# Kernel optimization log

Measured on AMD Instinct MI355X. Metric: run time of the kernel, lower is better.

## Reference

```python
import jax, jax.numpy as jnp
import numpy as np

B, S, HID = 2, 2048, 1024
H, HKV, D = 8, 2, 256
G = H // HKV            # GQA group size = 4
RD = D // 4             # partial rotary dim = 64
BASE = 10000000.0
EPS = 1e-6


def _rmsnorm(x, w):
    # x: [..., D]; matches QwenRMSNorm (fp32 math)
    xf = x.astype(jnp.float32)
    var = jnp.mean(xf * xf, axis=-1, keepdims=True)
    return w * (xf * jax.lax.rsqrt(var + EPS)).astype(x.dtype)


def _rotate_half(x):
    h = x.shape[-1] // 2
    return jnp.concatenate([-x[..., h:], x[..., :h]], axis=-1)


def _rope_cos_sin(position_ids, dtype):
    inv_freq = 1.0 / (BASE ** (jnp.arange(0, RD, 2, dtype=jnp.float32) / RD))
    freqs = position_ids.astype(jnp.float32)[:, None] * inv_freq[None, :]  # [S, RD/2]
    emb = jnp.concatenate([freqs, freqs], axis=-1)                          # [S, RD]
    return jnp.cos(emb).astype(dtype)[None, None], jnp.sin(emb).astype(dtype)[None, None]


def setup_inputs() -> dict:
    key = jax.random.key(0)
    ks = jax.random.split(key, 8)
    sc = lambda fan_in: 1.0 / np.sqrt(fan_in)
    return {
        "hidden_states": jax.random.normal(ks[0], (B, S, HID), jnp.float32),
        "position_ids": jnp.arange(S, dtype=jnp.int32),
        "Wq": jax.random.normal(ks[1], (H * D * 2, HID), jnp.float32) * sc(HID),
        "Wk": jax.random.normal(ks[2], (HKV * D, HID), jnp.float32) * sc(HID),
        "Wv": jax.random.normal(ks[3], (HKV * D, HID), jnp.float32) * sc(HID),
        "Wo": jax.random.normal(ks[4], (HID, H * D), jnp.float32) * sc(H * D),
        "q_norm_w": jnp.ones((D,), jnp.float32),
        "k_norm_w": jnp.ones((D,), jnp.float32),
    }


def reference(hidden_states, position_ids, Wq, Wk, Wv, Wo, q_norm_w, k_norm_w):
    b, s, _ = hidden_states.shape
    q_and_gate = hidden_states @ Wq.T                      # [B,S,2*H*D]
    q = q_and_gate[..., : H * D]
    gate = q_and_gate[..., H * D :]
    k = hidden_states @ Wk.T                               # [B,S,HKV*D]
    v = hidden_states @ Wv.T

    q = _rmsnorm(q.reshape(b, s, H, D), q_norm_w).transpose(0, 2, 1, 3)    # [B,H,S,D]
    k = _rmsnorm(k.reshape(b, s, HKV, D), k_norm_w).transpose(0, 2, 1, 3)  # [B,HKV,S,D]
    v = v.reshape(b, s, HKV, D).transpose(0, 2, 1, 3)                       # [B,HKV,S,D]

    cos, sin = _rope_cos_sin(position_ids, q.dtype)        # [1,1,S,RD]
    q_rot, q_pass = q[..., :RD], q[..., RD:]
    k_rot, k_pass = k[..., :RD], k[..., RD:]
    q = jnp.concatenate([q_rot * cos + _rotate_half(q_rot) * sin, q_pass], axis=-1)
    k = jnp.concatenate([k_rot * cos + _rotate_half(k_rot) * sin, k_pass], axis=-1)

    # GQA: group q heads by kv head instead of repeat_interleave (same math)
    qg = q.reshape(b, HKV, G, s, D)
    scale = 1.0 / np.sqrt(D).astype(np.float32)
    scores = jnp.einsum('bhgqd,bhkd->bhgqk', qg, k) * scale  # [B,HKV,G,S,S]
    attn = jax.nn.softmax(scores, axis=-1)                   # NOTE: no causal mask (as in source)
    out = jnp.einsum('bhgqk,bhkd->bhgqd', attn, v)           # [B,HKV,G,S,D]
    out = out.reshape(b, H, s, D).transpose(0, 2, 1, 3).reshape(b, s, H * D)

    out = out * jax.nn.silu(gate)
    return out @ Wo.T
```

## Files before the change

kernel.cpp:

```cpp
#include <hip/hip_runtime.h>
#include <math.h>

typedef unsigned short u16;
typedef unsigned int   u32;
typedef __attribute__((ext_vector_type(4))) float f32x4;
typedef __attribute__((ext_vector_type(8))) short s16x8;
typedef __attribute__((ext_vector_type(4))) unsigned short u16x4;

#define B_N   2
#define S_N   2048
#define HID_N 1024
#define H_N   8
#define HKV_N 2
#define D_N   256
#define QKVW  5120

__device__ __forceinline__ u16 f2bf(float f) {
  union { float f; u32 u; } x; x.f = f;
  u32 r = x.u + 0x7FFFu + ((x.u >> 16) & 1u);
  return (u16)(r >> 16);
}
__device__ __forceinline__ float bf2f(u16 u) {
  union { u32 u; float f; } x; x.u = ((u32)u) << 16; return x.f;
}
__device__ __forceinline__ void gload_lds16(const u16* g, u16* l) {
  __builtin_amdgcn_global_load_lds((const __attribute__((address_space(1))) u32*)g,
                                   (__attribute__((address_space(3))) u32*)l, 16, 0, 0);
}

__global__ __launch_bounds__(256)
void cast_bf16_kernel(const float* __restrict__ src, u16* __restrict__ dst, int n4) {
  int i = blockIdx.x * blockDim.x + threadIdx.x;
  int stride = gridDim.x * blockDim.x;
  for (; i < n4; i += stride) {
    float4 v = reinterpret_cast<const float4*>(src)[i];
    u16x4 o;
    o.x = f2bf(v.x); o.y = f2bf(v.y); o.z = f2bf(v.z); o.w = f2bf(v.w);
    reinterpret_cast<u16x4*>(dst)[i] = o;
  }
}

__global__ __launch_bounds__(256)
void trig_kernel(const int* __restrict__ pos, float* __restrict__ ct, float* __restrict__ st) {
  int i = blockIdx.x * blockDim.x + threadIdx.x;
  if (i >= S_N * 32) return;
  int s = i >> 5, j = i & 31;
  double inv = exp(-(double)j * (log(1.0e7) / 32.0));
  double ang = (double)pos[s] * inv;
  ct[i] = (float)cos(ang);
  st[i] = (float)sin(ang);
}

template <int OUT_BF16>
__global__ __launch_bounds__(256, 2)
void gemm_bt_kernel(const u16* __restrict__ A, const u16* __restrict__ Bw,
                    void* __restrict__ Cout, int M, int N, int K) {
  const int nbn = N >> 7;
  const int bm = blockIdx.x / nbn;
  const int bn = blockIdx.x % nbn;
  const int tid = threadIdx.x;
  const int lane = tid & 63;
  const int wr = tid >> 7;
  const int wc = (tid >> 6) & 1;
  __shared__ u16 sA[2][128 * 32];
  __shared__ u16 sB[2][128 * 32];
  f32x4 acc[4][4] = {};
  const u16* Ab = A + (size_t)(bm << 7) * K;
  const u16* Bb = Bw + (size_t)(bn << 7) * K;
  const int r_st = tid >> 2;
  const int c_st = (tid & 3) * 8;
  const int nkt = K >> 5;

  auto stage = [&](int buf, int kt) {
    const int k0 = kt << 5;
    gload_lds16(Ab + (size_t)r_st * K + k0 + c_st,        &sA[buf][tid * 8]);
    gload_lds16(Ab + (size_t)(r_st + 64) * K + k0 + c_st, &sA[buf][2048 + tid * 8]);
    gload_lds16(Bb + (size_t)r_st * K + k0 + c_st,        &sB[buf][tid * 8]);
    gload_lds16(Bb + (size_t)(r_st + 64) * K + k0 + c_st, &sB[buf][2048 + tid * 8]);
  };

  stage(0, 0);
  int cur = 0;
  const int ra = (wr << 6) + (lane & 15);
  const int rb = (wc << 6) + (lane & 15);
  const int ks = (lane >> 4) << 3;
  for (int kt = 0; kt < nkt; ++kt) {
    asm volatile("s_waitcnt vmcnt(0)" ::: "memory");
    __syncthreads();
    if (kt + 1 < nkt) stage(cur ^ 1, kt + 1);
    const u16* sa = sA[cur];
    const u16* sb = sB[cur];
    s16x8 af[4], bfr[4];
#pragma unroll
    for (int m = 0; m < 4; ++m) af[m] = *reinterpret_cast<const s16x8*>(sa + (ra + m * 16) * 32 + ks);
#pragma unroll
    for (int n = 0; n < 4; ++n) bfr[n] = *reinterpret_cast<const s16x8*>(sb + (rb + n * 16) * 32 + ks);
#pragma unroll
    for (int m = 0; m < 4; ++m)
#pragma unroll
      for (int n = 0; n < 4; ++n)
        acc[m][n] = __builtin_amdgcn_mfma_f32_16x16x32_bf16(af[m], bfr[n], acc[m][n], 0, 0, 0);
    cur ^= 1;
  }
  const int row0 = (bm << 7) + (wr << 6) + ((lane >> 4) << 2);
  const int col0 = (bn << 7) + (wc << 6) + (lane & 15);
#pragma unroll
  for (int m = 0; m < 4; ++m)
#pragma unroll
    for (int n = 0; n < 4; ++n)
#pragma unroll
      for (int j = 0; j < 4; ++j) {
        size_t idx = (size_t)(row0 + m * 16 + j) * N + col0 + n * 16;
        if (OUT_BF16) ((u16*)Cout)[idx] = f2bf(acc[m][n][j]);
        else          ((float*)Cout)[idx] = acc[m][n][j];
      }
}

__global__ __launch_bounds__(256)
void normrope_kernel(const u16* __restrict__ qkv, const float* __restrict__ qw,
                     const float* __restrict__ kw, const float* __restrict__ ct,
                     const float* __restrict__ st, u16* __restrict__ q_r,
                     u16* __restrict__ k_r) {
  const int lane = threadIdx.x & 63;
  const int row = blockIdx.x * 4 + (threadIdx.x >> 6);
  const int nq = B_N * S_N * H_N;
  const u16* src; u16* dst; const float* w;
  int s;
  if (row < nq) {
    int h = row & 7; int bs = row >> 3; s = bs & (S_N - 1); int b = bs >> 11;
    src = qkv + (size_t)(b * S_N + s) * QKVW + h * 256;
    dst = q_r + ((size_t)(b * H_N + h) * S_N + s) * 256;
    w = qw;
  } else {
    int r2 = row - nq;
    int h = r2 & 1; int bs = r2 >> 1; s = bs & (S_N - 1); int b = bs >> 11;
    src = qkv + (size_t)(b * S_N + s) * QKVW + 4096 + h * 256;
    dst = k_r + ((size_t)(b * HKV_N + h) * S_N + s) * 256;
    w = kw;
  }
  u16x4 xv = *reinterpret_cast<const u16x4*>(src + lane * 4);
  float x0 = bf2f(xv.x), x1 = bf2f(xv.y), x2 = bf2f(xv.z), x3 = bf2f(xv.w);
  float ss = x0 * x0 + x1 * x1 + x2 * x2 + x3 * x3;
#pragma unroll
  for (int off = 1; off < 64; off <<= 1) ss += __shfl_xor(ss, off);
  float rinv = rsqrtf(ss * (1.0f / 256.0f) + 1e-6f);
  float4 wv = *reinterpret_cast<const float4*>(w + lane * 4);
  float y[4] = { x0 * rinv * wv.x, x1 * rinv * wv.y, x2 * rinv * wv.z, x3 * rinv * wv.w };
  float p[4];
  p[0] = __shfl_xor(y[0], 8);
  p[1] = __shfl_xor(y[1], 8);
  p[2] = __shfl_xor(y[2], 8);
  p[3] = __shfl_xor(y[3], 8);
  if (lane < 16) {
    const float sgn = (lane < 8) ? -1.0f : 1.0f;
    const int jb = (lane * 4) & 31;
#pragma unroll
    for (int e = 0; e < 4; ++e) {
      float c = ct[(size_t)s * 32 + jb + e];
      float sn = st[(size_t)s * 32 + jb + e];
      y[e] = y[e] * c + sgn * p[e] * sn;
    }
  }
  u16x4 ov;
  ov.x = f2bf(y[0]); ov.y = f2bf(y[1]); ov.z = f2bf(y[2]); ov.w = f2bf(y[3]);
  *reinterpret_cast<u16x4*>(dst + lane * 4) = ov;
}

__global__ __launch_bounds__(256)
void vtrans_kernel(const u16* __restrict__ qkv, u16* __restrict__ vt) {
  const int bid = blockIdx.x;
  const int dt = bid & 3;
  const int stile = (bid >> 2) & 31;
  const int bh = bid >> 7;
  const int b = bh >> 1, kvh = bh & 1;
  __shared__ u16 tile[64][68];
  const int t = threadIdx.x;
  const u16* src = qkv + (size_t)(b * S_N + stile * 64) * QKVW + 4608 + kvh * 256 + dt * 64;
#pragma unroll
  for (int i = 0; i < 2; ++i) {
    int sl = i * 32 + (t >> 3);
    int d8 = (t & 7) * 8;
    s16x8 v = *reinterpret_cast<const s16x8*>(src + (size_t)sl * QKVW + d8);
    u16x4 lo = { (u16)v[0], (u16)v[1], (u16)v[2], (u16)v[3] };
    u16x4 hi = { (u16)v[4], (u16)v[5], (u16)v[6], (u16)v[7] };
    *reinterpret_cast<u16x4*>(&tile[sl][d8]) = lo;
    *reinterpret_cast<u16x4*>(&tile[sl][d8 + 4]) = hi;
  }
  __syncthreads();
#pragma unroll
  for (int i = 0; i < 2; ++i) {
    int dl = i * 32 + (t >> 3);
    int s8 = (t & 7) * 8;
    u16 tmp[8];
#pragma unroll
    for (int e = 0; e < 8; ++e) tmp[e] = tile[s8 + e][dl];
    u16x4 lo = { tmp[0], tmp[1], tmp[2], tmp[3] };
    u16x4 hi = { tmp[4], tmp[5], tmp[6], tmp[7] };
    u16* dstp = vt + ((size_t)(bh * 256 + dt * 64 + dl)) * S_N + stile * 64 + s8;
    *reinterpret_cast<u16x4*>(dstp) = lo;
    *reinterpret_cast<u16x4*>(dstp + 4) = hi;
  }
}

__global__ __launch_bounds__(512, 2)
void attn_kernel(const u16* __restrict__ q_r, const u16* __restrict__ k_r,
                 const u16* __restrict__ vt, const u16* __restrict__ qkv,
                 u16* __restrict__ act) {
  const int dd = blockIdx.x;
  const int xcd = dd & 7;
  const int idx = dd >> 3;
  const int combo = xcd >> 1;
  const int within = (xcd & 1) * 32 + idx;
  const int b = combo >> 1;
  const int kvh = combo & 1;
  const int h = kvh * 4 + (within >> 4);
  const int qt = within & 15;

  const int tid = threadIdx.x;
  const int lane = tid & 63;
  const int wv = tid >> 6;
  const int l15 = lane & 15;
  const int l4 = lane >> 4;

  __shared__ u16 sK[2][64 * 256];
  __shared__ u16 sVt[2][256 * 64];
  __shared__ u16 sP[8][16 * 64];

  const int q0 = qt * 128 + wv * 16;
  const u16* qb = q_r + ((size_t)(b * H_N + h) * S_N + q0) * 256;
  s16x8 qf[8];
#pragma unroll
  for (int kk = 0; kk < 8; ++kk)
    qf[kk] = *reinterpret_cast<const s16x8*>(qb + (size_t)l15 * 256 + kk * 32 + l4 * 8);

  f32x4 oacc[16] = {};
  float mrow[4] = { -1e30f, -1e30f, -1e30f, -1e30f };
  float lrow[4] = { 0.f, 0.f, 0.f, 0.f };

  const u16* kbase = k_r + ((size_t)(b * HKV_N + kvh) * S_N) * 256;
  const u16* vbase = vt + ((size_t)(b * HKV_N + kvh) * 256) * S_N;

  const int krow_b = tid >> 5;
  const int kp = tid & 31;
  const int vrow_b = tid >> 3;
  const int vp = tid & 7;

  auto stageKV = [&](int buf, int step) {
    const int kv0 = step << 6;
#pragma unroll
    for (int i = 0; i < 4; ++i) {
      const int krow = i * 16 + krow_b;
      gload_lds16(kbase + (size_t)(kv0 + krow) * 256 + ((kp ^ (krow_b & 7)) << 3),
                  &sK[buf][i * 4096 + tid * 8]);
    }
#pragma unroll
    for (int i = 0; i < 4; ++i) {
      const int vrow = i * 64 + vrow_b;
      gload_lds16(vbase + (size_t)vrow * S_N + kv0 + ((vp ^ (vrow_b & 7)) << 3),
                  &sVt[buf][i * 4096 + tid * 8]);
    }
  };

  stageKV(0, 0);
  int cur = 0;
  const float scale = 0.0625f;
  const int sw = (l15 & 7);
  for (int step = 0; step < 32; ++step) {
    asm volatile("s_waitcnt vmcnt(0)" ::: "memory");
    __syncthreads();
    if (step + 1 < 32) stageKV(cur ^ 1, step + 1);
    const u16* ktile = sK[cur];
    const u16* vtile = sVt[cur];

    f32x4 sacc[4] = {};
#pragma unroll
    for (int kk = 0; kk < 8; ++kk) {
      const int slot = kk * 4 + l4;
#pragma unroll
      for (int g = 0; g < 4; ++g) {
        const int row = g * 16 + l15;
        s16x8 kf = *reinterpret_cast<const s16x8*>(ktile + row * 256 + ((slot ^ sw) << 3));
        sacc[g] = __builtin_amdgcn_mfma_f32_16x16x32_bf16(qf[kk], kf, sacc[g], 0, 0, 0);
      }
    }

    float sc[16];
#pragma unroll
    for (int g = 0; g < 4; ++g)
#pragma unroll
      for (int j = 0; j < 4; ++j) sc[g * 4 + j] = sacc[g][j] * scale;
    float vmax[4];
#pragma unroll
    for (int j = 0; j < 4; ++j) {
      float v = fmaxf(fmaxf(sc[j], sc[4 + j]), fmaxf(sc[8 + j], sc[12 + j]));
      v = fmaxf(v, __shfl_xor(v, 1));
      v = fmaxf(v, __shfl_xor(v, 2));
      v = fmaxf(v, __shfl_xor(v, 4));
      v = fmaxf(v, __shfl_xor(v, 8));
      vmax[j] = v;
    }
    float grow = fmaxf(fmaxf(vmax[0] - mrow[0], vmax[1] - mrow[1]),
                       fmaxf(vmax[2] - mrow[2], vmax[3] - mrow[3]));
    if (__any(grow > 0.0f)) {
      float alpha[4];
#pragma unroll
      for (int j = 0; j < 4; ++j) {
        float mnew = fmaxf(mrow[j], vmax[j]);
        alpha[j] = __expf(mrow[j] - mnew);
        mrow[j] = mnew;
        lrow[j] *= alpha[j];
      }
#pragma unroll
      for (int nf = 0; nf < 16; ++nf) {
        oacc[nf][0] *= alpha[0]; oacc[nf][1] *= alpha[1];
        oacc[nf][2] *= alpha[2]; oacc[nf][3] *= alpha[3];
      }
    }
    float p[16];
#pragma unroll
    for (int g = 0; g < 4; ++g)
#pragma unroll
      for (int j = 0; j < 4; ++j) p[g * 4 + j] = __expf(sc[g * 4 + j] - mrow[j]);
#pragma unroll
    for (int j = 0; j < 4; ++j) {
      float r = (p[j] + p[4 + j]) + (p[8 + j] + p[12 + j]);
      r += __shfl_xor(r, 1);
      r += __shfl_xor(r, 2);
      r += __shfl_xor(r, 4);
      r += __shfl_xor(r, 8);
      lrow[j] += r;
    }

    u16* pl = &sP[wv][0];
#pragma unroll
    for (int g = 0; g < 4; ++g)
#pragma unroll
      for (int j = 0; j < 4; ++j) {
        const int row = l4 * 4 + j;
        const int col = g * 16 + l15;
        pl[row * 64 + ((((col >> 3) ^ (row & 7)) << 3) | (col & 7))] = f2bf(p[g * 4 + j]);
      }
    asm volatile("s_waitcnt lgkmcnt(0)" ::: "memory");
    __builtin_amdgcn_sched_barrier(0);

#pragma unroll
    for (int chunk = 0; chunk < 2; ++chunk) {
      s16x8 paf = *reinterpret_cast<const s16x8*>(
          pl + l15 * 64 + (((chunk * 4 + l4) ^ sw) << 3));
#pragma unroll
      for (int nf = 0; nf < 16; ++nf) {
        const int d = nf * 16 + l15;
        s16x8 vf = *reinterpret_cast<const s16x8*>(
            vtile + d * 64 + (((chunk * 4 + l4) ^ sw) << 3));
        oacc[nf] = __builtin_amdgcn_mfma_f32_16x16x32_bf16(paf, vf, oacc[nf], 0, 0, 0);
      }
    }
    cur ^= 1;
  }

  float invl[4];
#pragma unroll
  for (int j = 0; j < 4; ++j) invl[j] = 1.0f / lrow[j];
#pragma unroll
  for (int nf = 0; nf < 16; ++nf) {
#pragma unroll
    for (int j = 0; j < 4; ++j) {
      const int srow = q0 + l4 * 4 + j;
      const int d = nf * 16 + l15;
      float o = oacc[nf][j] * invl[j];
      float g = bf2f(qkv[(size_t)(b * S_N + srow) * QKVW + 2048 + h * 256 + d]);
      float sg = g / (1.0f + __expf(-g));
      act[(size_t)(b * S_N + srow) * 2048 + h * 256 + d] = f2bf(o * sg);
    }
  }
}

extern "C" void kernel_launch(void* const* d_in, const int* in_sizes, int n_in,
                              void* d_out, int out_size, void* d_ws, size_t ws_size,
                              hipStream_t stream) {
  const float* hs  = (const float*)d_in[0];
  const int*   pos = (const int*)d_in[1];
  const float* Wq  = (const float*)d_in[2];
  const float* Wk  = (const float*)d_in[3];
  const float* Wv  = (const float*)d_in[4];
  const float* Wo  = (const float*)d_in[5];
  const float* qw  = (const float*)d_in[6];
  const float* kw  = (const float*)d_in[7];
  float* out = (float*)d_out;

  char* w8 = (char*)d_ws;
  u16* hs_bf   = (u16*)(w8);
  u16* wqkv_bf = (u16*)(w8 + 8388608);
  u16* wo_bf   = (u16*)(w8 + 18874368);
  u16* qkv_raw = (u16*)(w8 + 23068672);
  u16* q_r     = (u16*)(w8 + 65011712);
  u16* k_r     = (u16*)(w8 + 81788928);
  u16* vt      = (u16*)(w8 + 85983232);
  u16* act     = (u16*)(w8 + 90177536);
  float* cost  = (float*)(w8 + 106954752);
  float* sint  = (float*)(w8 + 107216896);

  auto cast_launch = [&](const float* src, u16* dst, int n) {
    int n4 = n >> 2;
    int blocks = (n4 + 255) / 256;
    if (blocks > 2048) blocks = 2048;
    cast_bf16_kernel<<<blocks, 256, 0, stream>>>(src, dst, n4);
  };
  cast_launch(hs, hs_bf, B_N * S_N * HID_N);
  cast_launch(Wq, wqkv_bf, 4096 * 1024);
  cast_launch(Wk, wqkv_bf + 4194304, 512 * 1024);
  cast_launch(Wv, wqkv_bf + 4718592, 512 * 1024);
  cast_launch(Wo, wo_bf, 1024 * 2048);

  trig_kernel<<<(S_N * 32) / 256, 256, 0, stream>>>(pos, cost, sint);

  gemm_bt_kernel<1><<<32 * 40, 256, 0, stream>>>(hs_bf, wqkv_bf, (void*)qkv_raw, 4096, 5120, 1024);

  normrope_kernel<<<(B_N * S_N * (H_N + HKV_N)) / 4, 256, 0, stream>>>(
      qkv_raw, qw, kw, cost, sint, q_r, k_r);
  vtrans_kernel<<<512, 256, 0, stream>>>(qkv_raw, vt);

  attn_kernel<<<256, 512, 0, stream>>>(q_r, k_r, vt, qkv_raw, act);

  gemm_bt_kernel<0><<<32 * 8, 256, 0, stream>>>(act, wo_bf, (void*)out, 4096, 1024, 2048);
}
```

Measured before the change: 256.4 us.

## Restructure attention blocks so each wave covers one GQA head with 32 query rows

Each attention block now holds 4 waves, one per query head of a KV group, and each wave processes 32 query rows (two 16-row groups) over a shared 32-row query tile. Each K/V fragment read from LDS now feeds two MFMAs, which halves LDS read traffic per MFMA. MFMA sections are also wrapped in s_setprio raises. In exchange, per-thread registers double (oacc 2x16 accumulators) and occupancy drops to a single 256-thread block per CU, which reduces latency hiding.

```diff
diff --git a/kernel.cpp b/kernel.cpp
--- a/kernel.cpp
+++ b/kernel.cpp
@@ -202,7 +202,7 @@
   }
 }
 
-__global__ __launch_bounds__(512, 2)
+__global__ __launch_bounds__(256, 1)
 void attn_kernel(const u16* __restrict__ q_r, const u16* __restrict__ k_r,
                  const u16* __restrict__ vt, const u16* __restrict__ qkv,
                  u16* __restrict__ act) {
@@ -210,61 +210,66 @@
   const int xcd = dd & 7;
   const int idx = dd >> 3;
   const int combo = xcd >> 1;
-  const int within = (xcd & 1) * 32 + idx;
+  const int qt = (xcd & 1) * 32 + idx;
   const int b = combo >> 1;
   const int kvh = combo & 1;
-  const int h = kvh * 4 + (within >> 4);
-  const int qt = within & 15;
 
   const int tid = threadIdx.x;
   const int lane = tid & 63;
   const int wv = tid >> 6;
+  const int h = kvh * 4 + wv;
   const int l15 = lane & 15;
   const int l4 = lane >> 4;
 
   __shared__ u16 sK[2][64 * 256];
   __shared__ u16 sVt[2][256 * 64];
-  __shared__ u16 sP[8][16 * 64];
-
-  const int q0 = qt * 128 + wv * 16;
+  __shared__ u16 sP[4][32 * 64];
+
+  const int q0 = qt * 32;
   const u16* qb = q_r + ((size_t)(b * H_N + h) * S_N + q0) * 256;
-  s16x8 qf[8];
-#pragma unroll
-  for (int kk = 0; kk < 8; ++kk)
-    qf[kk] = *reinterpret_cast<const s16x8*>(qb + (size_t)l15 * 256 + kk * 32 + l4 * 8);
-
-  f32x4 oacc[16] = {};
-  float mrow[4] = { -1e30f, -1e30f, -1e30f, -1e30f };
-  float lrow[4] = { 0.f, 0.f, 0.f, 0.f };
+  s16x8 qf[2][8];
+#pragma unroll
+  for (int rg = 0; rg < 2; ++rg)
+#pragma unroll
+    for (int kk = 0; kk < 8; ++kk)
+      qf[rg][kk] = *reinterpret_cast<const s16x8*>(
+          qb + (size_t)(rg * 16 + l15) * 256 + kk * 32 + l4 * 8);
+
+  f32x4 oacc[2][16] = {};
+  float mrow[2][4], lrow[2][4];
+#pragma unroll
+  for (int rg = 0; rg < 2; ++rg)
+#pragma unroll
+    for (int j = 0; j < 4; ++j) { mrow[rg][j] = -1e30f; lrow[rg][j] = 0.f; }
 
   const u16* kbase = k_r + ((size_t)(b * HKV_N + kvh) * S_N) * 256;
   const u16* vbase = vt + ((size_t)(b * HKV_N + kvh) * 256) * S_N;
 
-  const int krow_b = tid >> 5;
-  const int kp = tid & 31;
-  const int vrow_b = tid >> 3;
-  const int vp = tid & 7;
+  const int k_sc = tid & 31;
+  const int k_rb = tid >> 5;
+  const int v_sc = tid & 7;
+  const int v_rb = (tid >> 3) & 7;
 
   auto stageKV = [&](int buf, int step) {
     const int kv0 = step << 6;
 #pragma unroll
-    for (int i = 0; i < 4; ++i) {
-      const int krow = i * 16 + krow_b;
-      gload_lds16(kbase + (size_t)(kv0 + krow) * 256 + ((kp ^ (krow_b & 7)) << 3),
-                  &sK[buf][i * 4096 + tid * 8]);
-    }
-#pragma unroll
-    for (int i = 0; i < 4; ++i) {
-      const int vrow = i * 64 + vrow_b;
-      gload_lds16(vbase + (size_t)vrow * S_N + kv0 + ((vp ^ (vrow_b & 7)) << 3),
-                  &sVt[buf][i * 4096 + tid * 8]);
+    for (int i = 0; i < 8; ++i) {
+      const int row = i * 8 + k_rb;
+      gload_lds16(kbase + (size_t)(kv0 + row) * 256 + ((k_sc ^ k_rb) << 3),
+                  &sK[buf][i * 2048 + tid * 8]);
+    }
+#pragma unroll
+    for (int i = 0; i < 8; ++i) {
+      const int rowd = i * 32 + (tid >> 3);
+      gload_lds16(vbase + (size_t)rowd * S_N + kv0 + ((v_sc ^ v_rb) << 3),
+                  &sVt[buf][i * 2048 + tid * 8]);
     }
   };
 
   stageKV(0, 0);
   int cur = 0;
   const float scale = 0.0625f;
-  const int sw = (l15 & 7);
+  const int sw = l15 & 7;
   for (int step = 0; step < 32; ++step) {
     asm volatile("s_waitcnt vmcnt(0)" ::: "memory");
     __syncthreads();
@@ -272,107 +277,135 @@
     const u16* ktile = sK[cur];
     const u16* vtile = sVt[cur];
 
-    f32x4 sacc[4] = {};
+    f32x4 sacc[2][4] = {};
+    __builtin_amdgcn_s_setprio(1);
 #pragma unroll
     for (int kk = 0; kk < 8; ++kk) {
       const int slot = kk * 4 + l4;
 #pragma unroll
       for (int g = 0; g < 4; ++g) {
-        const int row = g * 16 + l15;
-        s16x8 kf = *reinterpret_cast<const s16x8*>(ktile + row * 256 + ((slot ^ sw) << 3));
-        sacc[g] = __builtin_amdgcn_mfma_f32_16x16x32_bf16(qf[kk], kf, sacc[g], 0, 0, 0);
-      }
-    }
-
-    float sc[16];
-#pragma unroll
-    for (int g = 0; g < 4; ++g)
-#pragma unroll
-      for (int j = 0; j < 4; ++j) sc[g * 4 + j] = sacc[g][j] * scale;
-    float vmax[4];
-#pragma unroll
-    for (int j = 0; j < 4; ++j) {
-      float v = fmaxf(fmaxf(sc[j], sc[4 + j]), fmaxf(sc[8 + j], sc[12 + j]));
-      v = fmaxf(v, __shfl_xor(v, 1));
-      v = fmaxf(v, __shfl_xor(v, 2));
-      v = fmaxf(v, __shfl_xor(v, 4));
-      v = fmaxf(v, __shfl_xor(v, 8));
-      vmax[j] = v;
-    }
-    float grow = fmaxf(fmaxf(vmax[0] - mrow[0], vmax[1] - mrow[1]),
-                       fmaxf(vmax[2] - mrow[2], vmax[3] - mrow[3]));
+        s16x8 kf = *reinterpret_cast<const s16x8*>(
+            ktile + (g * 16 + l15) * 256 + ((slot ^ sw) << 3));
+        sacc[0][g] = __builtin_amdgcn_mfma_f32_16x16x32_bf16(qf[0][kk], kf, sacc[0][g], 0, 0, 0);
+        sacc[1][g] = __builtin_amdgcn_mfma_f32_16x16x32_bf16(qf[1][kk], kf, sacc[1][g], 0, 0, 0);
+      }
+    }
+    __builtin_amdgcn_s_setprio(0);
+
+    float sc[2][16];
+#pragma unroll
+    for (int rg = 0; rg < 2; ++rg)
+#pragma unroll
+      for (int g = 0; g < 4; ++g)
+#pragma unroll
+        for (int j = 0; j < 4; ++j) sc[rg][g * 4 + j] = sacc[rg][g][j] * scale;
+    float vmax[2][4];
+#pragma unroll
+    for (int rg = 0; rg < 2; ++rg)
+#pragma unroll
+      for (int j = 0; j < 4; ++j) {
+        float v = fmaxf(fmaxf(sc[rg][j], sc[rg][4 + j]),
+                        fmaxf(sc[rg][8 + j], sc[rg][12 + j]));
+        v = fmaxf(v, __shfl_xor(v, 1));
+        v = fmaxf(v, __shfl_xor(v, 2));
+        v = fmaxf(v, __shfl_xor(v, 4));
+        v = fmaxf(v, __shfl_xor(v, 8));
+        vmax[rg][j] = v;
+      }
+    float grow = -1.f;
+#pragma unroll
+    for (int rg = 0; rg < 2; ++rg)
+#pragma unroll
+      for (int j = 0; j < 4; ++j) grow = fmaxf(grow, vmax[rg][j] - mrow[rg][j]);
     if (__any(grow > 0.0f)) {
-      float alpha[4];
+#pragma unroll
+      for (int rg = 0; rg < 2; ++rg) {
+        float alpha[4];
+#pragma unroll
+        for (int j = 0; j < 4; ++j) {
+          float mnew = fmaxf(mrow[rg][j], vmax[rg][j]);
+          alpha[j] = __expf(mrow[rg][j] - mnew);
+          mrow[rg][j] = mnew;
+          lrow[rg][j] *= alpha[j];
+        }
+#pragma unroll
+        for (int nf = 0; nf < 16; ++nf) {
+          oacc[rg][nf][0] *= alpha[0]; oacc[rg][nf][1] *= alpha[1];
+          oacc[rg][nf][2] *= alpha[2]; oacc[rg][nf][3] *= alpha[3];
+        }
+      }
+    }
+    float p[2][16];
+#pragma unroll
+    for (int rg = 0; rg < 2; ++rg) {
+#pragma unroll
+      for (int g = 0; g < 4; ++g)
+#pragma unroll
+        for (int j = 0; j < 4; ++j)
+          p[rg][g * 4 + j] = __expf(sc[rg][g * 4 + j] - mrow[rg][j]);
 #pragma unroll
       for (int j = 0; j < 4; ++j) {
-        float mnew = fmaxf(mrow[j], vmax[j]);
-        alpha[j] = __expf(mrow[j] - mnew);
-        mrow[j] = mnew;
-        lrow[j] *= alpha[j];
-      }
-#pragma unroll
-      for (int nf = 0; nf < 16; ++nf) {
-        oacc[nf][0] *= alpha[0]; oacc[nf][1] *= alpha[1];
-        oacc[nf][2] *= alpha[2]; oacc[nf][3] *= alpha[3];
-      }
-    }
-    float p[16];
-#pragma unroll
-    for (int g = 0; g < 4; ++g)
-#pragma unroll
-      for (int j = 0; j < 4; ++j) p[g * 4 + j] = __expf(sc[g * 4 + j] - mrow[j]);
-#pragma unroll
-    for (int j = 0; j < 4; ++j) {
-      float r = (p[j] + p[4 + j]) + (p[8 + j] + p[12 + j]);
-      r += __shfl_xor(r, 1);
-      r += __shfl_xor(r, 2);
-      r += __shfl_xor(r, 4);
-      r += __shfl_xor(r, 8);
-      lrow[j] += r;
+        float r = (p[rg][j] + p[rg][4 + j]) + (p[rg][8 + j] + p[rg][12 + j]);
+        r += __shfl_xor(r, 1);
+        r += __shfl_xor(r, 2);
+        r += __shfl_xor(r, 4);
+        r += __shfl_xor(r, 8);
+        lrow[rg][j] += r;
+      }
     }
 
     u16* pl = &sP[wv][0];
 #pragma unroll
-    for (int g = 0; g < 4; ++g)
-#pragma unroll
-      for (int j = 0; j < 4; ++j) {
-        const int row = l4 * 4 + j;
-        const int col = g * 16 + l15;
-        pl[row * 64 + ((((col >> 3) ^ (row & 7)) << 3) | (col & 7))] = f2bf(p[g * 4 + j]);
-      }
+    for (int rg = 0; rg < 2; ++rg)
+#pragma unroll
+      for (int g = 0; g < 4; ++g)
+#pragma unroll
+        for (int j = 0; j < 4; ++j) {
+          const int row = rg * 16 + l4 * 4 + j;
+          const int col = g * 16 + l15;
+          pl[row * 64 + ((((col >> 3) ^ (row & 7)) << 3) | (col & 7))] = f2bf(p[rg][g * 4 + j]);
+        }
     asm volatile("s_waitcnt lgkmcnt(0)" ::: "memory");
     __builtin_amdgcn_sched_barrier(0);
 
-#pragma unroll
-    for (int chunk = 0; chunk < 2; ++chunk) {
-      s16x8 paf = *reinterpret_cast<const s16x8*>(
-          pl + l15 * 64 + (((chunk * 4 + l4) ^ sw) << 3));
+    __builtin_amdgcn_s_setprio(1);
+#pragma unroll
+    for (int c = 0; c < 2; ++c) {
+      s16x8 paf[2];
+#pragma unroll
+      for (int rg = 0; rg < 2; ++rg)
+        paf[rg] = *reinterpret_cast<const s16x8*>(
+            pl + (rg * 16 + l15) * 64 + (((c * 4 + l4) ^ sw) << 3));
 #pragma unroll
       for (int nf = 0; nf < 16; ++nf) {
+        s16x8 vf = *reinterpret_cast<const s16x8*>(
+            vtile + (nf * 16 + l15) * 64 + (((c * 4 + l4) ^ sw) << 3));
+        oacc[0][nf] = __builtin_amdgcn_mfma_f32_16x16x32_bf16(paf[0], vf, oacc[0][nf], 0, 0, 0);
+        oacc[1][nf] = __builtin_amdgcn_mfma_f32_16x16x32_bf16(paf[1], vf, oacc[1][nf], 0, 0, 0);
+      }
+    }
+    __builtin_amdgcn_s_setprio(0);
+    cur ^= 1;
+  }
+
+  float invl[2][4];
+#pragma unroll
+  for (int rg = 0; rg < 2; ++rg)
+#pragma unroll
+    for (int j = 0; j < 4; ++j) invl[rg][j] = 1.0f / lrow[rg][j];
+#pragma unroll
+  for (int rg = 0; rg < 2; ++rg)
+#pragma unroll
+    for (int nf = 0; nf < 16; ++nf)
+#pragma unroll
+      for (int j = 0; j < 4; ++j) {
+        const int srow = q0 + rg * 16 + l4 * 4 + j;
         const int d = nf * 16 + l15;
-        s16x8 vf = *reinterpret_cast<const s16x8*>(
-            vtile + d * 64 + (((chunk * 4 + l4) ^ sw) << 3));
-        oacc[nf] = __builtin_amdgcn_mfma_f32_16x16x32_bf16(paf, vf, oacc[nf], 0, 0, 0);
-      }
-    }
-    cur ^= 1;
-  }
-
-  float invl[4];
-#pragma unroll
-  for (int j = 0; j < 4; ++j) invl[j] = 1.0f / lrow[j];
-#pragma unroll
-  for (int nf = 0; nf < 16; ++nf) {
-#pragma unroll
-    for (int j = 0; j < 4; ++j) {
-      const int srow = q0 + l4 * 4 + j;
-      const int d = nf * 16 + l15;
-      float o = oacc[nf][j] * invl[j];
-      float g = bf2f(qkv[(size_t)(b * S_N + srow) * QKVW + 2048 + h * 256 + d]);
-      float sg = g / (1.0f + __expf(-g));
-      act[(size_t)(b * S_N + srow) * 2048 + h * 256 + d] = f2bf(o * sg);
-    }
-  }
+        float o = oacc[rg][nf][j] * invl[rg][j];
+        float g = bf2f(qkv[(size_t)(b * S_N + srow) * QKVW + 2048 + h * 256 + d]);
+        float sg = g / (1.0f + __expf(-g));
+        act[(size_t)(b * S_N + srow) * 2048 + h * 256 + d] = f2bf(o * sg);
+      }
 }
 
 extern "C" void kernel_launch(void* const* d_in, const int* in_sizes, int n_in,
@@ -420,7 +453,7 @@
       qkv_raw, qw, kw, cost, sint, q_r, k_r);
   vtrans_kernel<<<512, 256, 0, stream>>>(qkv_raw, vt);
 
-  attn_kernel<<<256, 512, 0, stream>>>(q_r, k_r, vt, qkv_raw, act);
+  attn_kernel<<<256, 256, 0, stream>>>(q_r, k_r, vt, qkv_raw, act);
 
   gemm_bt_kernel<0><<<32 * 8, 256, 0, stream>>>(act, wo_bf, (void*)out, 4096, 1024, 2048);
 }
```

Result: slower. 314.0 us (+22.5%).

## Transpose QK^T MFMA operands so each lane owns one query row for softmax

Applied to the files above, without the earlier changes.

Swaps the MFMA operand order in the score computation so the score tile is transposed and each lane holds scores for a single query row across 16 key columns. Row max and row sum then need only two cross-lane shuffles instead of four shuffles per row for four rows, and the running max and sum collapse to scalars. P is packed with v_cvt_pk_bf16_f32 and written as 8-byte vector stores through a new swizzle, and the scale is folded into an fma inside the exp. Rescale factors and the final normalizer are broadcast back to the accumulator layout with __shfl, which adds some cross-lane traffic.

```diff
diff --git a/kernel.cpp b/kernel.cpp
--- a/kernel.cpp
+++ b/kernel.cpp
@@ -22,6 +22,11 @@
 }
 __device__ __forceinline__ float bf2f(u16 u) {
   union { u32 u; float f; } x; x.u = ((u32)u) << 16; return x.f;
+}
+__device__ __forceinline__ u32 pk_bf16(float lo, float hi) {
+  u32 r;
+  asm("v_cvt_pk_bf16_f32 %0, %1, %2" : "=v"(r) : "v"(lo), "v"(hi));
+  return r;
 }
 __device__ __forceinline__ void gload_lds16(const u16* g, u16* l) {
   __builtin_amdgcn_global_load_lds((const __attribute__((address_space(1))) u32*)g,
@@ -234,8 +239,8 @@
     qf[kk] = *reinterpret_cast<const s16x8*>(qb + (size_t)l15 * 256 + kk * 32 + l4 * 8);
 
   f32x4 oacc[16] = {};
-  float mrow[4] = { -1e30f, -1e30f, -1e30f, -1e30f };
-  float lrow[4] = { 0.f, 0.f, 0.f, 0.f };
+  float mrow = -1e30f;
+  float lrow = 0.f;
 
   const u16* kbase = k_r + ((size_t)(b * HKV_N + kvh) * S_N) * 256;
   const u16* vbase = vt + ((size_t)(b * HKV_N + kvh) * 256) * S_N;
@@ -264,7 +269,8 @@
   stageKV(0, 0);
   int cur = 0;
   const float scale = 0.0625f;
-  const int sw = (l15 & 7);
+  const int sw = l15 & 7;
+  const int swp = l15 & 14;
   for (int step = 0; step < 32; ++step) {
     asm volatile("s_waitcnt vmcnt(0)" ::: "memory");
     __syncthreads();
@@ -278,96 +284,83 @@
       const int slot = kk * 4 + l4;
 #pragma unroll
       for (int g = 0; g < 4; ++g) {
-        const int row = g * 16 + l15;
-        s16x8 kf = *reinterpret_cast<const s16x8*>(ktile + row * 256 + ((slot ^ sw) << 3));
-        sacc[g] = __builtin_amdgcn_mfma_f32_16x16x32_bf16(qf[kk], kf, sacc[g], 0, 0, 0);
+        s16x8 kf = *reinterpret_cast<const s16x8*>(
+            ktile + (g * 16 + l15) * 256 + ((slot ^ sw) << 3));
+        sacc[g] = __builtin_amdgcn_mfma_f32_16x16x32_bf16(kf, qf[kk], sacc[g], 0, 0, 0);
       }
     }
 
-    float sc[16];
+    float vmax = sacc[0][0];
 #pragma unroll
     for (int g = 0; g < 4; ++g)
 #pragma unroll
-      for (int j = 0; j < 4; ++j) sc[g * 4 + j] = sacc[g][j] * scale;
-    float vmax[4];
-#pragma unroll
-    for (int j = 0; j < 4; ++j) {
-      float v = fmaxf(fmaxf(sc[j], sc[4 + j]), fmaxf(sc[8 + j], sc[12 + j]));
-      v = fmaxf(v, __shfl_xor(v, 1));
-      v = fmaxf(v, __shfl_xor(v, 2));
-      v = fmaxf(v, __shfl_xor(v, 4));
-      v = fmaxf(v, __shfl_xor(v, 8));
-      vmax[j] = v;
-    }
-    float grow = fmaxf(fmaxf(vmax[0] - mrow[0], vmax[1] - mrow[1]),
-                       fmaxf(vmax[2] - mrow[2], vmax[3] - mrow[3]));
-    if (__any(grow > 0.0f)) {
-      float alpha[4];
-#pragma unroll
-      for (int j = 0; j < 4; ++j) {
-        float mnew = fmaxf(mrow[j], vmax[j]);
-        alpha[j] = __expf(mrow[j] - mnew);
-        mrow[j] = mnew;
-        lrow[j] *= alpha[j];
+      for (int j = 0; j < 4; ++j) vmax = fmaxf(vmax, sacc[g][j]);
+    vmax = fmaxf(vmax, __shfl_xor(vmax, 16));
+    vmax = fmaxf(vmax, __shfl_xor(vmax, 32));
+    if (__any(vmax > mrow)) {
+      float mnew = fmaxf(mrow, vmax);
+      float alpha = __expf((mrow - mnew) * scale);
+      mrow = mnew;
+      lrow *= alpha;
+      float ab[4];
+#pragma unroll
+      for (int j = 0; j < 4; ++j) ab[j] = __shfl(alpha, l4 * 4 + j);
+#pragma unroll
+      for (int nf = 0; nf < 16; ++nf) {
+        oacc[nf][0] *= ab[0]; oacc[nf][1] *= ab[1];
+        oacc[nf][2] *= ab[2]; oacc[nf][3] *= ab[3];
       }
-#pragma unroll
-      for (int nf = 0; nf < 16; ++nf) {
-        oacc[nf][0] *= alpha[0]; oacc[nf][1] *= alpha[1];
-        oacc[nf][2] *= alpha[2]; oacc[nf][3] *= alpha[3];
-      }
-    }
+    }
+    const float msc = mrow * scale;
     float p[16];
 #pragma unroll
     for (int g = 0; g < 4; ++g)
 #pragma unroll
-      for (int j = 0; j < 4; ++j) p[g * 4 + j] = __expf(sc[g * 4 + j] - mrow[j]);
-#pragma unroll
-    for (int j = 0; j < 4; ++j) {
-      float r = (p[j] + p[4 + j]) + (p[8 + j] + p[12 + j]);
-      r += __shfl_xor(r, 1);
-      r += __shfl_xor(r, 2);
-      r += __shfl_xor(r, 4);
-      r += __shfl_xor(r, 8);
-      lrow[j] += r;
-    }
+      for (int j = 0; j < 4; ++j)
+        p[g * 4 + j] = __expf(fmaf(sacc[g][j], scale, -msc));
+    float r = ((p[0] + p[1]) + (p[2] + p[3])) + ((p[4] + p[5]) + (p[6] + p[7]))
+            + ((p[8] + p[9]) + (p[10] + p[11])) + ((p[12] + p[13]) + (p[14] + p[15]));
+    r += __shfl_xor(r, 16);
+    r += __shfl_xor(r, 32);
+    lrow += r;
 
     u16* pl = &sP[wv][0];
 #pragma unroll
-    for (int g = 0; g < 4; ++g)
-#pragma unroll
-      for (int j = 0; j < 4; ++j) {
-        const int row = l4 * 4 + j;
-        const int col = g * 16 + l15;
-        pl[row * 64 + ((((col >> 3) ^ (row & 7)) << 3) | (col & 7))] = f2bf(p[g * 4 + j]);
-      }
+    for (int g = 0; g < 4; ++g) {
+      u32 lo = pk_bf16(p[g * 4 + 0], p[g * 4 + 1]);
+      u32 hi = pk_bf16(p[g * 4 + 2], p[g * 4 + 3]);
+      union { u32 w[2]; u16x4 v; } u;
+      u.w[0] = lo; u.w[1] = hi;
+      *reinterpret_cast<u16x4*>(pl + l15 * 64 + (((g * 4 + l4) ^ swp) << 2)) = u.v;
+    }
     asm volatile("s_waitcnt lgkmcnt(0)" ::: "memory");
     __builtin_amdgcn_sched_barrier(0);
 
 #pragma unroll
-    for (int chunk = 0; chunk < 2; ++chunk) {
+    for (int c = 0; c < 2; ++c) {
       s16x8 paf = *reinterpret_cast<const s16x8*>(
-          pl + l15 * 64 + (((chunk * 4 + l4) ^ sw) << 3));
+          pl + l15 * 64 + (((c * 8 + l4 * 2) ^ swp) << 2));
 #pragma unroll
       for (int nf = 0; nf < 16; ++nf) {
-        const int d = nf * 16 + l15;
         s16x8 vf = *reinterpret_cast<const s16x8*>(
-            vtile + d * 64 + (((chunk * 4 + l4) ^ sw) << 3));
+            vtile + (nf * 16 + l15) * 64 + (((c * 4 + l4) ^ sw) << 3));
         oacc[nf] = __builtin_amdgcn_mfma_f32_16x16x32_bf16(paf, vf, oacc[nf], 0, 0, 0);
       }
     }
     cur ^= 1;
   }
 
-  float invl[4];
-#pragma unroll
-  for (int j = 0; j < 4; ++j) invl[j] = 1.0f / lrow[j];
+  float invl = 1.0f / lrow;
+  float ib[4];
+#pragma unroll
+  for (int j = 0; j < 4; ++j) ib[j] = __shfl(invl, l4 * 4 + j);
 #pragma unroll
   for (int nf = 0; nf < 16; ++nf) {
 #pragma unroll
     for (int j = 0; j < 4; ++j) {
       const int srow = q0 + l4 * 4 + j;
       const int d = nf * 16 + l15;
-      float o = oacc[nf][j] * invl[j];
+      float o = oacc[nf][j] * ib[j];
       float g = bf2f(qkv[(size_t)(b * S_N + srow) * QKVW + 2048 + h * 256 + d]);
       float sg = g / (1.0f + __expf(-g));
       act[(size_t)(b * S_N + srow) * 2048 + h * 256 + d] = f2bf(o * sg);
```

New measurement: 233.7 us. 1.1x faster.
